# Optimization experiments

Measured on AMD Instinct MI355X. Metric: run time of the kernel, lower is better.

Reference implementation:

```python
import jax, jax.numpy as jnp
import numpy as np


def setup_inputs() -> dict:
    key = jax.random.key(0)
    ks = jax.random.split(key, 6)
    B, Din, Dout, K, L = 4096, 4096, 4096, 256, 4
    # scale params like kaiming-ish init to keep activations O(1)
    hin = jax.random.normal(ks[0], (B, Din), dtype=jnp.float32)
    S1s = jax.random.normal(ks[1], (L, Din, K), dtype=jnp.float32) / np.sqrt(Din)
    S2s = jax.random.normal(ks[2], (L, K, Dout), dtype=jnp.float32) / np.sqrt(K)
    U1s = jax.random.normal(ks[3], (L, K, Dout), dtype=jnp.float32) / np.sqrt(K)
    U2s = jax.random.normal(ks[4], (L, Din, K), dtype=jnp.float32) / np.sqrt(Din)
    bias = jax.random.normal(ks[5], (Dout,), dtype=jnp.float32)
    return {"hin": hin, "S1s": S1s, "S2s": S2s, "U1s": U1s, "U2s": U2s, "bias": bias}


def reference(hin, S1s, S2s, U1s, U2s, bias):
    # out = (sum_l (hin @ S1s_l @ U1s_l + hin @ U2s_l @ S2s_l) + bias) / (2 L)
    L = S1s.shape[0]
    a = jnp.einsum('bd,ldk->lbk', hin, S1s)      # [L, B, K]
    t1 = jnp.einsum('lbk,lko->bo', a, U1s)       # [B, Dout]
    b = jnp.einsum('bd,ldk->lbk', hin, U2s)      # [L, B, K]
    t2 = jnp.einsum('lbk,lko->bo', b, S2s)       # [B, Dout]
    return (t1 + t2 + bias) / (2.0 * L)
```

## Files before the change

### kernel.cpp

```cpp
#include <hip/hip_runtime.h>
#include <stdint.h>

typedef unsigned short u16;
typedef __bf16 bf16x8 __attribute__((ext_vector_type(8)));
typedef float f32x4 __attribute__((ext_vector_type(4)));

#define DIN 4096
#define DOUT 4096
#define BB 4096
#define KR 256
#define RK 2048

__device__ __forceinline__ u16 f2bf(float f) {
    union { float f; unsigned u; } v; v.f = f;
    unsigned r = v.u + 0x7FFFu + ((v.u >> 16) & 1u);
    return (u16)(r >> 16);
}

__device__ __forceinline__ void gl_lds16(const void* g, void* l) {
    __builtin_amdgcn_global_load_lds((const __attribute__((address_space(1))) void*)g,
                                     (__attribute__((address_space(3))) void*)l,
                                     16, 0, 0);
}

__global__ __launch_bounds__(256) void cvt_f32_bf16(const float* __restrict__ src,
                                                    u16* __restrict__ dst, int n8) {
    int i = blockIdx.x * blockDim.x + threadIdx.x;
    if (i >= n8) return;
    const float4* s = reinterpret_cast<const float4*>(src) + (size_t)i * 2;
    float4 a = s[0], b = s[1];
    uint4 o;
    o.x = f2bf(a.x) | ((unsigned)f2bf(a.y) << 16);
    o.y = f2bf(a.z) | ((unsigned)f2bf(a.w) << 16);
    o.z = f2bf(b.x) | ((unsigned)f2bf(b.y) << 16);
    o.w = f2bf(b.z) | ((unsigned)f2bf(b.w) << 16);
    reinterpret_cast<uint4*>(dst)[i] = o;
}

__global__ __launch_bounds__(256) void pack_w1t(const float* __restrict__ S1s,
                                                const float* __restrict__ U2s,
                                                u16* __restrict__ W1T) {
    __shared__ u16 lds[64][68];
    int b  = blockIdx.x;
    int bd = b & 63;
    int bk = (b >> 6) & 3;
    int lb = b >> 8;
    int l = lb >> 1, br = lb & 1;
    const float* src = (br ? U2s : S1s) + (size_t)l * DIN * KR;
    int t = threadIdx.x;
    int d0 = bd * 64, k0 = bk * 64;
    int r0 = l * 512 + br * 256 + k0;
    #pragma unroll
    for (int p = 0; p < 4; ++p) {
        int dl = p * 16 + (t >> 4);
        int kc = (t & 15) * 4;
        float4 v = *reinterpret_cast<const float4*>(src + (size_t)(d0 + dl) * KR + k0 + kc);
        ushort4 pk;
        pk.x = f2bf(v.x); pk.y = f2bf(v.y); pk.z = f2bf(v.z); pk.w = f2bf(v.w);
        *reinterpret_cast<ushort4*>(&lds[dl][kc]) = pk;
    }
    __syncthreads();
    #pragma unroll
    for (int p = 0; p < 2; ++p) {
        int kl = p * 32 + (t >> 3);
        int d8 = t & 7;
        u16 tmp[8];
        #pragma unroll
        for (int j = 0; j < 8; ++j) tmp[j] = lds[d8 * 8 + j][kl];
        uint4 o;
        o.x = tmp[0] | ((unsigned)tmp[1] << 16);
        o.y = tmp[2] | ((unsigned)tmp[3] << 16);
        o.z = tmp[4] | ((unsigned)tmp[5] << 16);
        o.w = tmp[6] | ((unsigned)tmp[7] << 16);
        *reinterpret_cast<uint4*>(W1T + (size_t)(r0 + kl) * DIN + d0 + d8 * 8) = o;
    }
}

__global__ __launch_bounds__(256) void pack_w2t(const float* __restrict__ U1s,
                                                const float* __restrict__ S2s,
                                                u16* __restrict__ W2T) {
    __shared__ u16 lds[64][68];
    int b  = blockIdx.x;
    int bo = b & 63;
    int bk = (b >> 6) & 3;
    int lb = b >> 8;
    int l = lb >> 1, br = lb & 1;
    const float* src = (br ? S2s : U1s) + (size_t)l * KR * DOUT;
    int t = threadIdx.x;
    int o0 = bo * 64, k0 = bk * 64;
    #pragma unroll
    for (int p = 0; p < 4; ++p) {
        int kl = p * 16 + (t >> 4);
        int ol = (t & 15) * 4;
        float4 v = *reinterpret_cast<const float4*>(src + (size_t)(k0 + kl) * DOUT + o0 + ol);
        ushort4 pk;
        pk.x = f2bf(v.x); pk.y = f2bf(v.y); pk.z = f2bf(v.z); pk.w = f2bf(v.w);
        *reinterpret_cast<ushort4*>(&lds[kl][ol]) = pk;
    }
    __syncthreads();
    #pragma unroll
    for (int p = 0; p < 2; ++p) {
        int ol = p * 32 + (t >> 3);
        int k8 = t & 7;
        u16 tmp[8];
        #pragma unroll
        for (int j = 0; j < 8; ++j) tmp[j] = lds[k8 * 8 + j][ol];
        uint4 o;
        o.x = tmp[0] | ((unsigned)tmp[1] << 16);
        o.y = tmp[2] | ((unsigned)tmp[3] << 16);
        o.z = tmp[4] | ((unsigned)tmp[5] << 16);
        o.w = tmp[6] | ((unsigned)tmp[7] << 16);
        *reinterpret_cast<uint4*>(W2T + (size_t)(o0 + ol) * RK + l * 512 + br * 256 + k0 + k8 * 8) = o;
    }
}

template <int BN, int MW, int EPI>
__global__ __launch_bounds__(512)
__attribute__((amdgpu_waves_per_eu(2, 2)))
void gemm8(const u16* __restrict__ A,
           const u16* __restrict__ Bt,
           void* __restrict__ Cv,
           const float* __restrict__ bias,
           int N, int Kd) {
    extern __shared__ char smem[];
    constexpr int BHB = (BN == 256) ? 16384 : 8192;
    constexpr int BROWS = BN / 2;
    constexpr int NW = 8 / MW;
    constexpr int MF = 128 / (16 * MW);
    constexpr int MROW = 128 / MW;
    char* ldsA = smem;
    char* ldsB = smem + 65536;

    const int tid = threadIdx.x;
    const int l = tid & 63;
    const int wv = tid >> 6;
    const int wr = wv / NW;
    const int wc = wv % NW;

    int bid = blockIdx.x;
    bid = (bid & 7) * 32 + (bid >> 3);
    const int mt = bid >> 4, nt = bid & 15;
    const int m0 = mt * 256, n0 = nt * BN;

    const int NITER = Kd >> 7;

    unsigned aoff[2], boff[2];
    {
        #pragma unroll
        for (int r = 0; r < 2; ++r) {
            int lin = (r * 512 + tid) * 16;
            int s = lin ^ (((lin >> 7) & 7) << 4);
            int e = s >> 1;
            unsigned o = (unsigned)(e >> 6) * (unsigned)Kd + (unsigned)(e & 63);
            aoff[r] = (unsigned)m0 * (unsigned)Kd + o;
            boff[r] = (unsigned)n0 * (unsigned)Kd + o;
        }
    }

    auto issueA = [&](int h, int b, unsigned kb) {
        char* d = ldsA + (((b << 1) | h) * 16384) + tid * 16;
        gl_lds16(A + aoff[0] + (unsigned)h * 128u * (unsigned)Kd + kb, d);
        gl_lds16(A + aoff[1] + (unsigned)h * 128u * (unsigned)Kd + kb, d + 8192);
    };
    auto issueB = [&](int h, int b, unsigned kb) {
        char* d = ldsB + (((b << 1) | h) * BHB) + tid * 16;
        gl_lds16(Bt + boff[0] + (unsigned)h * (unsigned)BROWS * (unsigned)Kd + kb, d);
        if constexpr (BN == 256)
            gl_lds16(Bt + boff[1] + (unsigned)h * (unsigned)BROWS * (unsigned)Kd + kb, d + 8192);
    };

    const int cc0 = ((l >> 4) ^ (l & 7)) << 4;
    int rowAb[MF];
    #pragma unroll
    for (int m = 0; m < MF; ++m) rowAb[m] = ((wr * MROW + m * 16 + (l & 15)) * 128) | cc0;
    int rowBb[2];
    #pragma unroll
    for (int n = 0; n < 2; ++n) rowBb[n] = ((wc * 32 + n * 16 + (l & 15)) * 128) | cc0;

    f32x4 acc[2][2][MF][2] = {};
    bf16x8 afA[MF][2], afB[MF][2];
    bf16x8 bf0[2][2], bf1[2][2];

#define RDA(SET, B_, H_) do { const char* Ah_ = ldsA + (((B_) << 1) | (H_)) * 16384;  \
    _Pragma("unroll") for (int m_ = 0; m_ < MF; ++m_) {                               \
        SET[m_][0] = *(const bf16x8*)(Ah_ + rowAb[m_]);                               \
        SET[m_][1] = *(const bf16x8*)(Ah_ + (rowAb[m_] ^ 64)); } } while (0)
#define RDB(DST, B_, H_) do { const char* Bh_ = ldsB + (((B_) << 1) | (H_)) * BHB;    \
    _Pragma("unroll") for (int n_ = 0; n_ < 2; ++n_) {                                \
        DST[n_][0] = *(const bf16x8*)(Bh_ + rowBb[n_]);                               \
        DST[n_][1] = *(const bf16x8*)(Bh_ + (rowBb[n_] ^ 64)); } } while (0)
#define MM(MH, NH, ASET, BREG) do {                                                   \
    __builtin_amdgcn_s_setprio(1);                                                    \
    _Pragma("unroll") for (int m_ = 0; m_ < MF; ++m_)                                 \
        _Pragma("unroll") for (int n_ = 0; n_ < 2; ++n_) {                            \
            acc[MH][NH][m_][n_] = __builtin_amdgcn_mfma_f32_16x16x32_bf16(            \
                ASET[m_][0], BREG[n_][0], acc[MH][NH][m_][n_], 0, 0, 0);              \
            acc[MH][NH][m_][n_] = __builtin_amdgcn_mfma_f32_16x16x32_bf16(            \
                ASET[m_][1], BREG[n_][1], acc[MH][NH][m_][n_], 0, 0, 0); }            \
    __builtin_amdgcn_s_setprio(0); } while (0)
#define SB0 __builtin_amdgcn_sched_barrier(0)
#define VMW do { if constexpr (BN == 256)                                             \
                     asm volatile("s_waitcnt vmcnt(8)" ::: "memory");                 \
                 else asm volatile("s_waitcnt vmcnt(6)" ::: "memory"); } while (0)
#define ENDP do { asm volatile("" ::: "memory");                                      \
                  __builtin_amdgcn_s_barrier(); } while (0)

    issueA(0, 0, 0);  issueB(0, 0, 0);  issueB(1, 0, 0);  issueA(1, 0, 0);
    issueA(0, 1, 64); issueB(0, 1, 64); issueB(1, 1, 64); issueA(1, 1, 64);
    VMW;
    __builtin_amdgcn_s_barrier();
    RDA(afA, 0, 0);
    RDB(bf0, 0, 0);

    for (int J = 0; J < NITER; ++J) {
        const unsigned kb0 = ((unsigned)J << 7) + 128;
        const unsigned kb1 = kb0 + 64;
        issueA(0, 0, kb0); RDB(bf1, 0, 1); SB0; MM(0, 0, afA, bf0); ENDP;
        issueB(0, 0, kb0); RDA(afB, 0, 1); SB0; MM(0, 1, afA, bf1); VMW; ENDP;
        issueB(1, 0, kb0); RDA(afA, 1, 0); SB0; MM(1, 1, afB, bf1); ENDP;
        issueA(1, 0, kb0); MM(1, 0, afB, bf0); RDB(bf0, 1, 0); VMW; ENDP;
        issueA(0, 1, kb1); RDB(bf1, 1, 1); SB0; MM(0, 0, afA, bf0); ENDP;
        issueB(0, 1, kb1); RDA(afB, 1, 1); SB0; MM(0, 1, afA, bf1); VMW; ENDP;
        issueB(1, 1, kb1); RDA(afA, 0, 0); SB0; MM(1, 1, afB, bf1); ENDP;
        issueA(1, 1, kb1); MM(1, 0, afB, bf0); RDB(bf0, 0, 0); VMW; ENDP;
    }
#undef RDA
#undef RDB
#undef MM
#undef SB0
#undef VMW
#undef ENDP

    const int colc = l & 15, rb = (l >> 4) * 4;
    #pragma unroll
    for (int mh = 0; mh < 2; ++mh)
    #pragma unroll
    for (int nh = 0; nh < 2; ++nh)
    #pragma unroll
    for (int m = 0; m < MF; ++m)
    #pragma unroll
    for (int n = 0; n < 2; ++n) {
        int c = n0 + nh * (BN / 2) + wc * 32 + n * 16 + colc;
        int r0r = m0 + mh * 128 + wr * MROW + m * 16 + rb;
        if (EPI == 0) {
            u16* Cb = (u16*)Cv;
            #pragma unroll
            for (int j = 0; j < 4; ++j)
                Cb[(size_t)(r0r + j) * N + c] = f2bf(acc[mh][nh][m][n][j]);
        } else {
            float* Cf = (float*)Cv;
            float bv = bias[c];
            #pragma unroll
            for (int j = 0; j < 4; ++j)
                Cf[(size_t)(r0r + j) * N + c] = (acc[mh][nh][m][n][j] + bv) * 0.125f;
        }
    }
}

extern "C" void kernel_launch(void* const* d_in, const int* in_sizes, int n_in,
                              void* d_out, int out_size, void* d_ws, size_t ws_size,
                              hipStream_t stream) {
    const float* hin  = (const float*)d_in[0];
    const float* S1s  = (const float*)d_in[1];
    const float* S2s  = (const float*)d_in[2];
    const float* U1s  = (const float*)d_in[3];
    const float* U2s  = (const float*)d_in[4];
    const float* bias = (const float*)d_in[5];
    float* out = (float*)d_out;

    const size_t SZ_HIN = (size_t)BB * DIN * 2 + 512;
    const size_t SZ_W   = (size_t)RK * DIN * 2 + 512;
    const size_t SZ_A   = (size_t)BB * RK * 2 + 512;
    if (ws_size < SZ_HIN + SZ_W + SZ_A) return;
    u16* hinbf = (u16*)d_ws;
    u16* Wx    = (u16*)((char*)d_ws + SZ_HIN);
    u16* abf   = (u16*)((char*)d_ws + SZ_HIN + SZ_W);

    (void)hipFuncSetAttribute(reinterpret_cast<const void*>(&gemm8<128, 4, 0>),
                              hipFuncAttributeMaxDynamicSharedMemorySize, 98304);
    (void)hipFuncSetAttribute(reinterpret_cast<const void*>(&gemm8<256, 2, 1>),
                              hipFuncAttributeMaxDynamicSharedMemorySize, 131072);

    pack_w1t<<<64 * 4 * 8, 256, 0, stream>>>(S1s, U2s, Wx);
    cvt_f32_bf16<<<(BB * DIN / 8) / 256, 256, 0, stream>>>(hin, hinbf, BB * DIN / 8);
    gemm8<128, 4, 0><<<256, 512, 98304, stream>>>(hinbf, Wx, abf, nullptr, RK, DIN);
    pack_w2t<<<64 * 4 * 8, 256, 0, stream>>>(U1s, S2s, Wx);
    gemm8<256, 2, 1><<<256, 512, 131072, stream>>>(abf, Wx, out, bias, DOUT, RK);
}
```

Measured before the change: 201.5 us.

## Restructure GEMM main loop with deeper prefetch and per-GEMM pipeline variants

Reorders the 8-phase main loop so global-to-LDS loads for quarter-tiles are issued earlier, at a different phase offset. The vmcnt waits are relaxed to match the new number of outstanding loads. A PIPE template parameter selects between two LDS-read schedules: one reads A/B fragments just before use with a single A register set, the other double-buffers fragments across phases. The first GEMM uses the double-buffered variant and the second GEMM the simpler one. The sched_barrier hints are removed, so the compiler gets more freedom but the instruction ordering becomes less predictable.

```diff
diff --git a/kernel.cpp b/kernel.cpp
--- a/kernel.cpp
+++ b/kernel.cpp
@@ -114,7 +114,7 @@
     }
 }
 
-template <int BN, int MW, int EPI>
+template <int BN, int MW, int EPI, int PIPE>
 __global__ __launch_bounds__(512)
 __attribute__((amdgpu_waves_per_eu(2, 2)))
 void gemm8(const u16* __restrict__ A,
@@ -198,36 +198,47 @@
             acc[MH][NH][m_][n_] = __builtin_amdgcn_mfma_f32_16x16x32_bf16(            \
                 ASET[m_][1], BREG[n_][1], acc[MH][NH][m_][n_], 0, 0, 0); }            \
     __builtin_amdgcn_s_setprio(0); } while (0)
-#define SB0 __builtin_amdgcn_sched_barrier(0)
 #define VMW do { if constexpr (BN == 256)                                             \
-                     asm volatile("s_waitcnt vmcnt(8)" ::: "memory");                 \
-                 else asm volatile("s_waitcnt vmcnt(6)" ::: "memory"); } while (0)
+                     asm volatile("s_waitcnt vmcnt(4)" ::: "memory");                 \
+                 else asm volatile("s_waitcnt vmcnt(3)" ::: "memory"); } while (0)
 #define ENDP do { asm volatile("" ::: "memory");                                      \
                   __builtin_amdgcn_s_barrier(); } while (0)
 
-    issueA(0, 0, 0);  issueB(0, 0, 0);  issueB(1, 0, 0);  issueA(1, 0, 0);
-    issueA(0, 1, 64); issueB(0, 1, 64); issueB(1, 1, 64); issueA(1, 1, 64);
+    issueA(0, 0, 0);  issueB(0, 0, 0);
+    issueA(1, 0, 0);  issueB(1, 0, 0);
+    issueA(0, 1, 64); issueB(0, 1, 64);
     VMW;
     __builtin_amdgcn_s_barrier();
-    RDA(afA, 0, 0);
-    RDB(bf0, 0, 0);
-
-    for (int J = 0; J < NITER; ++J) {
-        const unsigned kb0 = ((unsigned)J << 7) + 128;
-        const unsigned kb1 = kb0 + 64;
-        issueA(0, 0, kb0); RDB(bf1, 0, 1); SB0; MM(0, 0, afA, bf0); ENDP;
-        issueB(0, 0, kb0); RDA(afB, 0, 1); SB0; MM(0, 1, afA, bf1); VMW; ENDP;
-        issueB(1, 0, kb0); RDA(afA, 1, 0); SB0; MM(1, 1, afB, bf1); ENDP;
-        issueA(1, 0, kb0); MM(1, 0, afB, bf0); RDB(bf0, 1, 0); VMW; ENDP;
-        issueA(0, 1, kb1); RDB(bf1, 1, 1); SB0; MM(0, 0, afA, bf0); ENDP;
-        issueB(0, 1, kb1); RDA(afB, 1, 1); SB0; MM(0, 1, afA, bf1); VMW; ENDP;
-        issueB(1, 1, kb1); RDA(afA, 0, 0); SB0; MM(1, 1, afB, bf1); ENDP;
-        issueA(1, 1, kb1); MM(1, 0, afB, bf0); RDB(bf0, 0, 0); VMW; ENDP;
+
+    if constexpr (PIPE == 0) {
+        for (int J = 0; J < NITER; ++J) {
+            const unsigned kc = ((unsigned)J << 7);
+            issueA(1, 1, kc + 64); RDA(afA, 0, 0); RDB(bf0, 0, 0); MM(0, 0, afA, bf0); ENDP;
+            issueB(1, 1, kc + 64); RDB(bf1, 0, 1); MM(0, 1, afA, bf1); ENDP;
+            issueA(0, 0, kc + 128); RDA(afA, 0, 1); MM(1, 1, afA, bf1); ENDP;
+            issueB(0, 0, kc + 128); MM(1, 0, afA, bf0); VMW; ENDP;
+            issueA(1, 0, kc + 128); RDA(afA, 1, 0); RDB(bf0, 1, 0); MM(0, 0, afA, bf0); ENDP;
+            issueB(1, 0, kc + 128); RDB(bf1, 1, 1); MM(0, 1, afA, bf1); ENDP;
+            issueA(0, 1, kc + 192); RDA(afA, 1, 1); MM(1, 1, afA, bf1); ENDP;
+            issueB(0, 1, kc + 192); MM(1, 0, afA, bf0); VMW; ENDP;
+        }
+    } else {
+        RDA(afA, 0, 0); RDB(bf0, 0, 0);
+        for (int J = 0; J < NITER; ++J) {
+            const unsigned kc = ((unsigned)J << 7);
+            issueA(1, 1, kc + 64); RDB(bf1, 0, 1); MM(0, 0, afA, bf0); ENDP;
+            issueB(1, 1, kc + 64); RDA(afB, 0, 1); MM(0, 1, afA, bf1); ENDP;
+            issueA(0, 0, kc + 128); MM(1, 1, afB, bf1); ENDP;
+            issueB(0, 0, kc + 128); MM(1, 0, afB, bf0); VMW; RDA(afA, 1, 0); RDB(bf0, 1, 0); ENDP;
+            issueA(1, 0, kc + 128); RDB(bf1, 1, 1); MM(0, 0, afA, bf0); ENDP;
+            issueB(1, 0, kc + 128); RDA(afB, 1, 1); MM(0, 1, afA, bf1); ENDP;
+            issueA(0, 1, kc + 192); MM(1, 1, afB, bf1); ENDP;
+            issueB(0, 1, kc + 192); MM(1, 0, afB, bf0); VMW; RDA(afA, 0, 0); RDB(bf0, 0, 0); ENDP;
+        }
     }
 #undef RDA
 #undef RDB
 #undef MM
-#undef SB0
 #undef VMW
 #undef ENDP
 
@@ -276,14 +287,14 @@
     u16* Wx    = (u16*)((char*)d_ws + SZ_HIN);
     u16* abf   = (u16*)((char*)d_ws + SZ_HIN + SZ_W);
 
-    (void)hipFuncSetAttribute(reinterpret_cast<const void*>(&gemm8<128, 4, 0>),
+    (void)hipFuncSetAttribute(reinterpret_cast<const void*>(&gemm8<128, 4, 0, 1>),
                               hipFuncAttributeMaxDynamicSharedMemorySize, 98304);
-    (void)hipFuncSetAttribute(reinterpret_cast<const void*>(&gemm8<256, 2, 1>),
+    (void)hipFuncSetAttribute(reinterpret_cast<const void*>(&gemm8<256, 2, 1, 0>),
                               hipFuncAttributeMaxDynamicSharedMemorySize, 131072);
 
     pack_w1t<<<64 * 4 * 8, 256, 0, stream>>>(S1s, U2s, Wx);
     cvt_f32_bf16<<<(BB * DIN / 8) / 256, 256, 0, stream>>>(hin, hinbf, BB * DIN / 8);
-    gemm8<128, 4, 0><<<256, 512, 98304, stream>>>(hinbf, Wx, abf, nullptr, RK, DIN);
+    gemm8<128, 4, 0, 1><<<256, 512, 98304, stream>>>(hinbf, Wx, abf, nullptr, RK, DIN);
     pack_w2t<<<64 * 4 * 8, 256, 0, stream>>>(U1s, S2s, Wx);
-    gemm8<256, 2, 1><<<256, 512, 131072, stream>>>(abf, Wx, out, bias, DOUT, RK);
-}
+    gemm8<256, 2, 1, 0><<<256, 512, 131072, stream>>>(abf, Wx, out, bias, DOUT, RK);
+}
```

Result: faster. 167.4 us (-16.9%).

## Restructure GEMM main loop into barrier-gated phases with single A fragment set

Applied to the files above, without the earlier changes.

Rewrites the software-pipelined GEMM loop so each phase reads LDS fragments, issues one global-to-LDS stage, then uses an s_barrier plus an lgkmcnt wait before its MFMAs. The previous double A-register set (afA/afB) becomes a single set, freeing registers. The prefetch order shifts by one stage, and the vmcnt thresholds are lowered to match. GEMM dimensions become template constants so address math can fold. This adds a second barrier per phase and removes the overlap of LDS reads with MFMAs, which may expose LDS latency.

```diff
diff --git a/kernel.cpp b/kernel.cpp
--- a/kernel.cpp
+++ b/kernel.cpp
@@ -114,14 +114,13 @@
     }
 }
 
-template <int BN, int MW, int EPI>
+template <int BN, int MW, int EPI, int ND, int KD>
 __global__ __launch_bounds__(512)
 __attribute__((amdgpu_waves_per_eu(2, 2)))
-void gemm8(const u16* __restrict__ A,
+void gemm9(const u16* __restrict__ A,
            const u16* __restrict__ Bt,
            void* __restrict__ Cv,
-           const float* __restrict__ bias,
-           int N, int Kd) {
+           const float* __restrict__ bias) {
     extern __shared__ char smem[];
     constexpr int BHB = (BN == 256) ? 16384 : 8192;
     constexpr int BROWS = BN / 2;
@@ -142,7 +141,7 @@
     const int mt = bid >> 4, nt = bid & 15;
     const int m0 = mt * 256, n0 = nt * BN;
 
-    const int NITER = Kd >> 7;
+    constexpr int NITER = KD >> 7;
 
     unsigned aoff[2], boff[2];
     {
@@ -151,22 +150,22 @@
             int lin = (r * 512 + tid) * 16;
             int s = lin ^ (((lin >> 7) & 7) << 4);
             int e = s >> 1;
-            unsigned o = (unsigned)(e >> 6) * (unsigned)Kd + (unsigned)(e & 63);
-            aoff[r] = (unsigned)m0 * (unsigned)Kd + o;
-            boff[r] = (unsigned)n0 * (unsigned)Kd + o;
+            unsigned o = (unsigned)(e >> 6) * (unsigned)KD + (unsigned)(e & 63);
+            aoff[r] = (unsigned)m0 * (unsigned)KD + o;
+            boff[r] = (unsigned)n0 * (unsigned)KD + o;
         }
     }
 
     auto issueA = [&](int h, int b, unsigned kb) {
         char* d = ldsA + (((b << 1) | h) * 16384) + tid * 16;
-        gl_lds16(A + aoff[0] + (unsigned)h * 128u * (unsigned)Kd + kb, d);
-        gl_lds16(A + aoff[1] + (unsigned)h * 128u * (unsigned)Kd + kb, d + 8192);
+        gl_lds16(A + aoff[0] + (unsigned)h * 128u * KD + kb, d);
+        gl_lds16(A + aoff[1] + (unsigned)h * 128u * KD + kb, d + 8192);
     };
     auto issueB = [&](int h, int b, unsigned kb) {
         char* d = ldsB + (((b << 1) | h) * BHB) + tid * 16;
-        gl_lds16(Bt + boff[0] + (unsigned)h * (unsigned)BROWS * (unsigned)Kd + kb, d);
+        gl_lds16(Bt + boff[0] + (unsigned)h * (unsigned)BROWS * KD + kb, d);
         if constexpr (BN == 256)
-            gl_lds16(Bt + boff[1] + (unsigned)h * (unsigned)BROWS * (unsigned)Kd + kb, d + 8192);
+            gl_lds16(Bt + boff[1] + (unsigned)h * (unsigned)BROWS * KD + kb, d + 8192);
     };
 
     const int cc0 = ((l >> 4) ^ (l & 7)) << 4;
@@ -178,58 +177,60 @@
     for (int n = 0; n < 2; ++n) rowBb[n] = ((wc * 32 + n * 16 + (l & 15)) * 128) | cc0;
 
     f32x4 acc[2][2][MF][2] = {};
-    bf16x8 afA[MF][2], afB[MF][2];
+    bf16x8 afA[MF][2];
     bf16x8 bf0[2][2], bf1[2][2];
 
-#define RDA(SET, B_, H_) do { const char* Ah_ = ldsA + (((B_) << 1) | (H_)) * 16384;  \
+#define RDA(B_, H_) do { const char* Ah_ = ldsA + (((B_) << 1) | (H_)) * 16384;       \
     _Pragma("unroll") for (int m_ = 0; m_ < MF; ++m_) {                               \
-        SET[m_][0] = *(const bf16x8*)(Ah_ + rowAb[m_]);                               \
-        SET[m_][1] = *(const bf16x8*)(Ah_ + (rowAb[m_] ^ 64)); } } while (0)
+        afA[m_][0] = *(const bf16x8*)(Ah_ + rowAb[m_]);                               \
+        afA[m_][1] = *(const bf16x8*)(Ah_ + (rowAb[m_] ^ 64)); } } while (0)
 #define RDB(DST, B_, H_) do { const char* Bh_ = ldsB + (((B_) << 1) | (H_)) * BHB;    \
     _Pragma("unroll") for (int n_ = 0; n_ < 2; ++n_) {                                \
         DST[n_][0] = *(const bf16x8*)(Bh_ + rowBb[n_]);                               \
         DST[n_][1] = *(const bf16x8*)(Bh_ + (rowBb[n_] ^ 64)); } } while (0)
-#define MM(MH, NH, ASET, BREG) do {                                                   \
+#define MM(MH, NH, BREG) do {                                                         \
     __builtin_amdgcn_s_setprio(1);                                                    \
     _Pragma("unroll") for (int m_ = 0; m_ < MF; ++m_)                                 \
         _Pragma("unroll") for (int n_ = 0; n_ < 2; ++n_) {                            \
             acc[MH][NH][m_][n_] = __builtin_amdgcn_mfma_f32_16x16x32_bf16(            \
-                ASET[m_][0], BREG[n_][0], acc[MH][NH][m_][n_], 0, 0, 0);              \
+                afA[m_][0], BREG[n_][0], acc[MH][NH][m_][n_], 0, 0, 0);               \
             acc[MH][NH][m_][n_] = __builtin_amdgcn_mfma_f32_16x16x32_bf16(            \
-                ASET[m_][1], BREG[n_][1], acc[MH][NH][m_][n_], 0, 0, 0); }            \
+                afA[m_][1], BREG[n_][1], acc[MH][NH][m_][n_], 0, 0, 0); }             \
     __builtin_amdgcn_s_setprio(0); } while (0)
-#define SB0 __builtin_amdgcn_sched_barrier(0)
 #define VMW do { if constexpr (BN == 256)                                             \
-                     asm volatile("s_waitcnt vmcnt(8)" ::: "memory");                 \
-                 else asm volatile("s_waitcnt vmcnt(6)" ::: "memory"); } while (0)
-#define ENDP do { asm volatile("" ::: "memory");                                      \
-                  __builtin_amdgcn_s_barrier(); } while (0)
+                     asm volatile("s_waitcnt vmcnt(6)" ::: "memory");                 \
+                 else asm volatile("s_waitcnt vmcnt(4)" ::: "memory"); } while (0)
+#define PH(RDS, STG, HINT, MH, NH, BREG, GATE) do {                                   \
+    RDS; STG;                                                                         \
+    if ((HINT) && BN == 256) asm volatile("s_waitcnt lgkmcnt(8)" ::: "memory");       \
+    __builtin_amdgcn_s_barrier();                                                     \
+    asm volatile("s_waitcnt lgkmcnt(0)" ::: "memory");                                \
+    MM(MH, NH, BREG);                                                                 \
+    if (GATE) VMW;                                                                    \
+    __builtin_amdgcn_s_barrier();                                                     \
+} while (0)
 
     issueA(0, 0, 0);  issueB(0, 0, 0);  issueB(1, 0, 0);  issueA(1, 0, 0);
-    issueA(0, 1, 64); issueB(0, 1, 64); issueB(1, 1, 64); issueA(1, 1, 64);
+    issueA(0, 1, 64); issueB(0, 1, 64); issueB(1, 1, 64);
     VMW;
     __builtin_amdgcn_s_barrier();
-    RDA(afA, 0, 0);
-    RDB(bf0, 0, 0);
 
     for (int J = 0; J < NITER; ++J) {
-        const unsigned kb0 = ((unsigned)J << 7) + 128;
-        const unsigned kb1 = kb0 + 64;
-        issueA(0, 0, kb0); RDB(bf1, 0, 1); SB0; MM(0, 0, afA, bf0); ENDP;
-        issueB(0, 0, kb0); RDA(afB, 0, 1); SB0; MM(0, 1, afA, bf1); VMW; ENDP;
-        issueB(1, 0, kb0); RDA(afA, 1, 0); SB0; MM(1, 1, afB, bf1); ENDP;
-        issueA(1, 0, kb0); MM(1, 0, afB, bf0); RDB(bf0, 1, 0); VMW; ENDP;
-        issueA(0, 1, kb1); RDB(bf1, 1, 1); SB0; MM(0, 0, afA, bf0); ENDP;
-        issueB(0, 1, kb1); RDA(afB, 1, 1); SB0; MM(0, 1, afA, bf1); VMW; ENDP;
-        issueB(1, 1, kb1); RDA(afA, 0, 0); SB0; MM(1, 1, afB, bf1); ENDP;
-        issueA(1, 1, kb1); MM(1, 0, afB, bf0); RDB(bf0, 0, 0); VMW; ENDP;
+        const unsigned kc = (unsigned)J << 7;
+        PH({ RDA(0, 0); RDB(bf0, 0, 0); }, issueA(1, 1, kc + 64),  1, 0, 0, bf0, 0);
+        PH({ RDB(bf1, 0, 1); },            issueA(0, 0, kc + 128), 0, 0, 1, bf1, 0);
+        PH({ RDA(0, 1); },                 issueB(0, 0, kc + 128), 0, 1, 1, bf1, 0);
+        PH({},                             issueB(1, 0, kc + 128), 0, 1, 0, bf0, 1);
+        PH({ RDA(1, 0); RDB(bf0, 1, 0); }, issueA(1, 0, kc + 128), 1, 0, 0, bf0, 0);
+        PH({ RDB(bf1, 1, 1); },            issueA(0, 1, kc + 192), 0, 0, 1, bf1, 0);
+        PH({ RDA(1, 1); },                 issueB(0, 1, kc + 192), 0, 1, 1, bf1, 0);
+        PH({},                             issueB(1, 1, kc + 192), 0, 1, 0, bf0, 1);
     }
 #undef RDA
 #undef RDB
 #undef MM
-#undef SB0
 #undef VMW
-#undef ENDP
+#undef PH
 
     const int colc = l & 15, rb = (l >> 4) * 4;
     #pragma unroll
@@ -246,13 +247,13 @@
             u16* Cb = (u16*)Cv;
             #pragma unroll
             for (int j = 0; j < 4; ++j)
-                Cb[(size_t)(r0r + j) * N + c] = f2bf(acc[mh][nh][m][n][j]);
+                Cb[(size_t)(r0r + j) * ND + c] = f2bf(acc[mh][nh][m][n][j]);
         } else {
             float* Cf = (float*)Cv;
             float bv = bias[c];
             #pragma unroll
             for (int j = 0; j < 4; ++j)
-                Cf[(size_t)(r0r + j) * N + c] = (acc[mh][nh][m][n][j] + bv) * 0.125f;
+                Cf[(size_t)(r0r + j) * ND + c] = (acc[mh][nh][m][n][j] + bv) * 0.125f;
         }
     }
 }
@@ -276,14 +277,14 @@
     u16* Wx    = (u16*)((char*)d_ws + SZ_HIN);
     u16* abf   = (u16*)((char*)d_ws + SZ_HIN + SZ_W);
 
-    (void)hipFuncSetAttribute(reinterpret_cast<const void*>(&gemm8<128, 4, 0>),
+    (void)hipFuncSetAttribute(reinterpret_cast<const void*>(&gemm9<128, 4, 0, RK, DIN>),
                               hipFuncAttributeMaxDynamicSharedMemorySize, 98304);
-    (void)hipFuncSetAttribute(reinterpret_cast<const void*>(&gemm8<256, 2, 1>),
+    (void)hipFuncSetAttribute(reinterpret_cast<const void*>(&gemm9<256, 2, 1, DOUT, RK>),
                               hipFuncAttributeMaxDynamicSharedMemorySize, 131072);
 
     pack_w1t<<<64 * 4 * 8, 256, 0, stream>>>(S1s, U2s, Wx);
     cvt_f32_bf16<<<(BB * DIN / 8) / 256, 256, 0, stream>>>(hin, hinbf, BB * DIN / 8);
-    gemm8<128, 4, 0><<<256, 512, 98304, stream>>>(hinbf, Wx, abf, nullptr, RK, DIN);
+    gemm9<128, 4, 0, RK, DIN><<<256, 512, 98304, stream>>>(hinbf, Wx, abf, nullptr);
     pack_w2t<<<64 * 4 * 8, 256, 0, stream>>>(U1s, S2s, Wx);
-    gemm8<256, 2, 1><<<256, 512, 131072, stream>>>(abf, Wx, out, bias, DOUT, RK);
-}
+    gemm9<256, 2, 1, DOUT, RK><<<256, 512, 131072, stream>>>(abf, Wx, out, bias);
+}
```

Result: faster. 165.9 us (-17.7%).
